# Kernel optimization log

Measured on AMD Instinct MI355X. Metric: run time of the kernel, lower is better.

The kernel has to match this reference:

```python
import jax, jax.numpy as jnp
import numpy as np

NUM_CLASSES = 4
SIGMA_S = 1.0
SIGMA_Z = 1.0


def _rbf_gram(x, sigma):
    # x: [N, d] -> [N, N] Gaussian kernel exp(-||xi-xj||^2 / (2 sigma^2))
    sq = jnp.sum(x * x, axis=-1)
    d2 = sq[:, None] + sq[None, :] - 2.0 * (x @ x.T)
    d2 = jnp.maximum(d2, 0.0)
    return jnp.exp(-d2 / (2.0 * sigma * sigma))


def _double_center(K):
    # Faithful to: K = mean_center(K, dim=0); K_m = mean_center(K.t(), dim=0)
    K = K - jnp.mean(K, axis=0, keepdims=True)
    K = K.T
    K = K - jnp.mean(K, axis=0, keepdims=True)
    return K


def setup_inputs() -> dict:
    key = jax.random.key(0)
    kz, ks = jax.random.split(key)
    z = jax.random.normal(kz, (8192, 128), dtype=jnp.float32)
    s = jax.random.randint(ks, (8192,), 0, NUM_CLASSES, dtype=jnp.int64)
    norm = jnp.float32(1.0)
    return {"z": z, "s": s, "norm": norm}


def reference(z, s, norm):
    n = z.shape[0]
    s_onehot = jax.nn.one_hot(s, NUM_CLASSES, dtype=z.dtype)  # format_onehot
    K_sm = _double_center(_rbf_gram(s_onehot, SIGMA_S))
    K_zm = _double_center(_rbf_gram(z, SIGMA_Z))
    # trace(K_zm.T @ K_sm) == sum(K_zm * K_sm): O(N^2) instead of O(N^3)
    dep = jnp.sum(K_zm * K_sm)
    dep = dep / (norm * (n * n))
    return dep
```

## Files before the change

kernel.cpp:

```cpp
#include <hip/hip_runtime.h>
#include <hip/hip_bf16.h>

typedef short bf16x8 __attribute__((ext_vector_type(8)));
typedef float f32x4  __attribute__((ext_vector_type(4)));

#define ZD      128
#define BT      128
#define D2_CUT  60.0f
#define D2_TRIG 62.0f

__device__ __forceinline__ unsigned short f2bf(float x) {
    unsigned u = __float_as_uint(x);
    u = (u + 0x7FFFu + ((u >> 16) & 1u)) >> 16;
    return (unsigned short)u;
}

__global__ __launch_bounds__(256) void dep_prep(
    const float* __restrict__ z, const int* __restrict__ s,
    float* __restrict__ sq, float* __restrict__ sqmin,
    unsigned short* __restrict__ zb, int* __restrict__ counts)
{
    __shared__ float part[64][33];
    const int tid  = threadIdx.x;
    const int wave = tid >> 6, lane = tid & 63;
    const int half = lane >> 5, c = lane & 31;
    const int r0   = blockIdx.x * 64;

    if (wave == 0) {
        int sv = s[r0 + lane];
        #pragma unroll
        for (int cl = 0; cl < 4; ++cl) {
            unsigned long long m = __ballot(sv == cl);
            if (lane == 0) atomicAdd(&counts[cl], __popcll(m));
        }
    }

    #pragma unroll
    for (int i = 0; i < 8; ++i) {
        const int rloc = wave * 16 + i * 2 + half;
        const int r    = r0 + rloc;
        float4 v = ((const float4*)z)[r * 32 + c];
        ushort4 u;
        u.x = f2bf(v.x); u.y = f2bf(v.y); u.z = f2bf(v.z); u.w = f2bf(v.w);
        ((ushort4*)zb)[r * 32 + c] = u;
        part[rloc][c] = v.x*v.x + v.y*v.y + v.z*v.z + v.w*v.w;
    }
    __syncthreads();

    if (wave == 0) {
        float sum = 0.f;
        #pragma unroll
        for (int k = 0; k < 32; ++k) sum += part[lane][k];
        sq[r0 + lane] = sum;
        float mn = sum;
        #pragma unroll
        for (int off = 1; off < 64; off <<= 1)
            mn = fminf(mn, __shfl_xor(mn, off, 64));
        if (lane == 0) sqmin[blockIdx.x] = mn;
    }
}

__global__ __launch_bounds__(256, 2) void dep_pair(
    const unsigned short* __restrict__ zb, const float* __restrict__ sq,
    const float* __restrict__ sqmin, const int* __restrict__ s,
    const int* __restrict__ counts, float* __restrict__ acc_out,
    int T, float invN)
{
    __shared__ unsigned short Apan[BT * ZD];
    __shared__ unsigned short Bpan[BT * ZD];

    const int tid = threadIdx.x;

    const int t = blockIdx.x;
    #define TRI_BASE(x) ((x) * T - ((x) * ((x) - 1)) / 2)
    double disc = (2.0 * T + 1.0) * (2.0 * T + 1.0) - 8.0 * (double)t;
    int ti = (int)((2.0 * T + 1.0 - sqrt(disc)) * 0.5);
    if (ti < 0) ti = 0;
    if (ti > T - 1) ti = T - 1;
    while (ti + 1 < T && TRI_BASE(ti + 1) <= t) ++ti;
    while (ti > 0 && TRI_BASE(ti) > t) --ti;
    const int tj = ti + (t - TRI_BASE(ti));
    #undef TRI_BASE

    const int i0 = ti * BT, j0 = tj * BT;

    #pragma unroll
    for (int i = 0; i < 8; ++i) {
        const int L   = i * 256 + tid;
        const int row = L >> 4, ch = L & 15;
        const int dst = row * ZD + (((ch ^ (row & 15)) << 3));
        uint4 a = ((const uint4*)(zb + (size_t)i0 * ZD))[L];
        uint4 b = ((const uint4*)(zb + (size_t)j0 * ZD))[L];
        *(uint4*)(Apan + dst) = a;
        *(uint4*)(Bpan + dst) = b;
    }
    __syncthreads();

    const int wave = tid >> 6, lane = tid & 63;
    const int wi = wave >> 1, wj = wave & 1;
    const int l15 = lane & 15, quad = lane >> 4;

    f32x4 accv[4][4];
    #pragma unroll
    for (int a = 0; a < 4; ++a)
        #pragma unroll
        for (int b = 0; b < 4; ++b)
            accv[a][b] = (f32x4){0.f, 0.f, 0.f, 0.f};

    #pragma unroll
    for (int kc = 0; kc < 4; ++kc) {
        bf16x8 af[4], bfr[4];
        #pragma unroll
        for (int it = 0; it < 4; ++it) {
            const int row = wi * 64 + it * 16 + l15;
            const int ch  = (quad + 4 * kc) ^ l15;
            af[it] = *(const bf16x8*)(Apan + row * ZD + (ch << 3));
        }
        #pragma unroll
        for (int jt = 0; jt < 4; ++jt) {
            const int row = wj * 64 + jt * 16 + l15;
            const int ch  = (quad + 4 * kc) ^ l15;
            bfr[jt] = *(const bf16x8*)(Bpan + row * ZD + (ch << 3));
        }
        #pragma unroll
        for (int it = 0; it < 4; ++it)
            #pragma unroll
            for (int jt = 0; jt < 4; ++jt)
                accv[it][jt] = __builtin_amdgcn_mfma_f32_16x16x32_bf16(
                    af[it], bfr[jt], accv[it][jt], 0, 0, 0);
    }

    float m = -1e30f;
    #pragma unroll
    for (int it = 0; it < 4; ++it)
        #pragma unroll
        for (int jt = 0; jt < 4; ++jt) {
            const f32x4 v = accv[it][jt];
            m = fmaxf(m, fmaxf(fmaxf(v[0], v[1]), fmaxf(v[2], v[3])));
        }
    #pragma unroll
    for (int off = 1; off < 64; off <<= 1)
        m = fmaxf(m, __shfl_xor(m, off, 64));

    const int gA = ti * 2 + wi, gB = tj * 2 + wj;
    const float bound = sqmin[gA] + sqmin[gB] - 2.0f * m;

    if (bound < D2_TRIG) {
        float p[4];
        #pragma unroll
        for (int cl = 0; cl < 4; ++cl) p[cl] = (float)counts[cl] * invN;
        const float sump2 = p[0]*p[0] + p[1]*p[1] + p[2]*p[2] + p[3]*p[3];

        const int ibase = i0 + wi * 64, jbase = j0 + wj * 64;
        float sqj[4];
        #pragma unroll
        for (int jt = 0; jt < 4; ++jt) sqj[jt] = sq[jbase + jt * 16 + l15];

        float local = 0.f;
        #pragma unroll
        for (int it = 0; it < 4; ++it) {
            #pragma unroll
            for (int r = 0; r < 4; ++r) {
                const int i = ibase + it * 16 + quad * 4 + r;
                const float sqi = sq[i];
                #pragma unroll
                for (int jt = 0; jt < 4; ++jt) {
                    const int j = jbase + jt * 16 + l15;
                    float d2 = sqi + sqj[jt] - 2.0f * accv[it][jt][r];
                    d2 = fmaxf(d2, 0.0f);
                    if (d2 < D2_CUT && i != j) {
                        const int si = s[i], sj = s[j];
                        const float w = (si == sj ? 1.0f : 0.0f)
                                      - p[si] - p[sj] + sump2;
                        local += w * __expf(-0.5f * d2);
                    }
                }
            }
        }
        if (ti < tj) local *= 2.0f;

        #pragma unroll
        for (int off = 32; off > 0; off >>= 1)
            local += __shfl_down(local, off, 64);
        if (lane == 0 && local != 0.0f)
            atomicAdd(acc_out, local);
    }
}

__global__ __launch_bounds__(64) void dep_finalize(
    const float* __restrict__ acc, const int* __restrict__ counts,
    const float* __restrict__ norm, float* __restrict__ out, int N)
{
    if (threadIdx.x == 0) {
        double n  = (double)N;
        double c2 = 0.0;
        for (int cl = 0; cl < 4; ++cl)
            c2 += (double)counts[cl] * (double)counts[cl];
        double diag  = n - c2 / n;
        double total = ((double)acc[0] + diag) * (1.0 - exp(-1.0));
        out[0] = (float)(total / ((double)norm[0] * n * n));
    }
}

extern "C" void kernel_launch(void* const* d_in, const int* in_sizes, int n_in,
                              void* d_out, int out_size, void* d_ws, size_t ws_size,
                              hipStream_t stream)
{
    const float* z    = (const float*)d_in[0];
    const int*   s    = (const int*)d_in[1];
    const float* norm = (const float*)d_in[2];
    float* out = (float*)d_out;

    const int N = in_sizes[1];
    const int T = N / BT;

    char* ws = (char*)d_ws;
    float* acc    = (float*)ws;
    int*   counts = (int*)(ws + 16);
    float* sq     = (float*)(ws + 64);
    float* sqmin  = (float*)(ws + 64 + (size_t)N * 4);
    unsigned short* zb =
        (unsigned short*)(ws + 64 + (size_t)N * 4 + (size_t)(N / 64) * 4 + 48);

    hipMemsetAsync(d_ws, 0, 64, stream);
    dep_prep<<<N / 64, 256, 0, stream>>>(z, s, sq, sqmin, zb, counts);

    const int nblocks = T * (T + 1) / 2;
    dep_pair<<<nblocks, 256, 0, stream>>>(zb, sq, sqmin, s, counts, acc,
                                          T, 1.0f / (float)N);
    dep_finalize<<<1, 64, 0, stream>>>(acc, counts, norm, out, N);
}
```

Before: 87.11 us.

## Drop A-panel LDS, fuse finalize via last-block counter, remove memset

The pair kernel no longer stages the A tile in shared memory. Each wave loads its A fragments straight from global memory, double-buffered across k-chunks, which halves LDS use and lets launch bounds rise to three blocks per SM. The memset and the finalize kernel are removed: the prep kernel zeroes the accumulator and writes per-block class counts instead of using atomics, and the last pair block, found through an atomic done counter, computes the final value. This saves two launches and LDS pressure, at the cost of uncoalesced global A loads, extra register pressure, and a loop over all per-block counts in every active block.

```diff
diff --git a/kernel.cpp b/kernel.cpp
--- a/kernel.cpp
+++ b/kernel.cpp
@@ -18,7 +18,8 @@
 __global__ __launch_bounds__(256) void dep_prep(
     const float* __restrict__ z, const int* __restrict__ s,
     float* __restrict__ sq, float* __restrict__ sqmin,
-    unsigned short* __restrict__ zb, int* __restrict__ counts)
+    unsigned short* __restrict__ zb, int* __restrict__ counts4,
+    float* __restrict__ acc, unsigned int* __restrict__ done)
 {
     __shared__ float part[64][33];
     const int tid  = threadIdx.x;
@@ -26,12 +27,14 @@
     const int half = lane >> 5, c = lane & 31;
     const int r0   = blockIdx.x * 64;
 
+    if (blockIdx.x == 0 && tid == 192) { *acc = 0.0f; *done = 0u; }
+
     if (wave == 0) {
         int sv = s[r0 + lane];
         #pragma unroll
         for (int cl = 0; cl < 4; ++cl) {
             unsigned long long m = __ballot(sv == cl);
-            if (lane == 0) atomicAdd(&counts[cl], __popcll(m));
+            if (lane == 0) counts4[blockIdx.x * 4 + cl] = __popcll(m);
         }
     }
 
@@ -60,13 +63,14 @@
     }
 }
 
-__global__ __launch_bounds__(256, 2) void dep_pair(
+__global__ __launch_bounds__(256, 3) void dep_pair(
     const unsigned short* __restrict__ zb, const float* __restrict__ sq,
     const float* __restrict__ sqmin, const int* __restrict__ s,
-    const int* __restrict__ counts, float* __restrict__ acc_out,
-    int T, float invN)
+    const int* __restrict__ counts4, int nPrep,
+    float* __restrict__ acc, unsigned int* __restrict__ done,
+    const float* __restrict__ norm, float* __restrict__ out,
+    int T, int N, float invN)
 {
-    __shared__ unsigned short Apan[BT * ZD];
     __shared__ unsigned short Bpan[BT * ZD];
 
     const int tid = threadIdx.x;
@@ -83,22 +87,29 @@
     #undef TRI_BASE
 
     const int i0 = ti * BT, j0 = tj * BT;
+    const int wave = tid >> 6, lane = tid & 63;
+    const int wi = wave >> 1, wj = wave & 1;
+    const int l15 = lane & 15, quad = lane >> 4;
 
     #pragma unroll
     for (int i = 0; i < 8; ++i) {
         const int L   = i * 256 + tid;
         const int row = L >> 4, ch = L & 15;
         const int dst = row * ZD + (((ch ^ (row & 15)) << 3));
-        uint4 a = ((const uint4*)(zb + (size_t)i0 * ZD))[L];
-        uint4 b = ((const uint4*)(zb + (size_t)j0 * ZD))[L];
-        *(uint4*)(Apan + dst) = a;
-        *(uint4*)(Bpan + dst) = b;
-    }
+        *(uint4*)(Bpan + dst) = ((const uint4*)(zb + (size_t)j0 * ZD))[L];
+    }
+
+    const unsigned short* abase[4];
+    #pragma unroll
+    for (int it = 0; it < 4; ++it)
+        abase[it] = zb + (size_t)(i0 + wi * 64 + it * 16 + l15) * ZD + quad * 8;
+
+    bf16x8 af[2][4];
+    #pragma unroll
+    for (int it = 0; it < 4; ++it)
+        af[0][it] = *(const bf16x8*)(abase[it]);
+
     __syncthreads();
-
-    const int wave = tid >> 6, lane = tid & 63;
-    const int wi = wave >> 1, wj = wave & 1;
-    const int l15 = lane & 15, quad = lane >> 4;
 
     f32x4 accv[4][4];
     #pragma unroll
@@ -109,13 +120,13 @@
 
     #pragma unroll
     for (int kc = 0; kc < 4; ++kc) {
-        bf16x8 af[4], bfr[4];
-        #pragma unroll
-        for (int it = 0; it < 4; ++it) {
-            const int row = wi * 64 + it * 16 + l15;
-            const int ch  = (quad + 4 * kc) ^ l15;
-            af[it] = *(const bf16x8*)(Apan + row * ZD + (ch << 3));
-        }
+        if (kc < 3) {
+            #pragma unroll
+            for (int it = 0; it < 4; ++it)
+                af[(kc + 1) & 1][it] =
+                    *(const bf16x8*)(abase[it] + (kc + 1) * 32);
+        }
+        bf16x8 bfr[4];
         #pragma unroll
         for (int jt = 0; jt < 4; ++jt) {
             const int row = wj * 64 + jt * 16 + l15;
@@ -127,7 +138,7 @@
             #pragma unroll
             for (int jt = 0; jt < 4; ++jt)
                 accv[it][jt] = __builtin_amdgcn_mfma_f32_16x16x32_bf16(
-                    af[it], bfr[jt], accv[it][jt], 0, 0, 0);
+                    af[kc & 1][it], bfr[jt], accv[it][jt], 0, 0, 0);
     }
 
     float m = -1e30f;
@@ -146,9 +157,16 @@
     const float bound = sqmin[gA] + sqmin[gB] - 2.0f * m;
 
     if (bound < D2_TRIG) {
+        int cnt[4] = {0, 0, 0, 0};
+        for (int b = 0; b < nPrep; ++b) {
+            cnt[0] += counts4[b * 4 + 0];
+            cnt[1] += counts4[b * 4 + 1];
+            cnt[2] += counts4[b * 4 + 2];
+            cnt[3] += counts4[b * 4 + 3];
+        }
         float p[4];
         #pragma unroll
-        for (int cl = 0; cl < 4; ++cl) p[cl] = (float)counts[cl] * invN;
+        for (int cl = 0; cl < 4; ++cl) p[cl] = (float)cnt[cl] * invN;
         const float sump2 = p[0]*p[0] + p[1]*p[1] + p[2]*p[2] + p[3]*p[3];
 
         const int ibase = i0 + wi * 64, jbase = j0 + wj * 64;
@@ -183,22 +201,25 @@
         for (int off = 32; off > 0; off >>= 1)
             local += __shfl_down(local, off, 64);
         if (lane == 0 && local != 0.0f)
-            atomicAdd(acc_out, local);
-    }
-}
-
-__global__ __launch_bounds__(64) void dep_finalize(
-    const float* __restrict__ acc, const int* __restrict__ counts,
-    const float* __restrict__ norm, float* __restrict__ out, int N)
-{
-    if (threadIdx.x == 0) {
-        double n  = (double)N;
-        double c2 = 0.0;
-        for (int cl = 0; cl < 4; ++cl)
-            c2 += (double)counts[cl] * (double)counts[cl];
-        double diag  = n - c2 / n;
-        double total = ((double)acc[0] + diag) * (1.0 - exp(-1.0));
-        out[0] = (float)(total / ((double)norm[0] * n * n));
+            atomicAdd(acc, local);
+    }
+
+    __syncthreads();
+    if (tid == 0) {
+        __threadfence();
+        if (atomicAdd(done, 1u) == (unsigned)gridDim.x - 1u) {
+            float a = atomicAdd(acc, 0.0f);
+            double c2 = 0.0;
+            for (int cl = 0; cl < 4; ++cl) {
+                long long cc = 0;
+                for (int b = 0; b < nPrep; ++b) cc += counts4[b * 4 + cl];
+                c2 += (double)cc * (double)cc;
+            }
+            double n     = (double)N;
+            double diag  = n - c2 / n;
+            double total = ((double)a + diag) * (1.0 - exp(-1.0));
+            out[0] = (float)(total / ((double)norm[0] * n * n));
+        }
     }
 }
 
@@ -213,20 +234,21 @@
 
     const int N = in_sizes[1];
     const int T = N / BT;
+    const int nPrep = N / 64;
 
     char* ws = (char*)d_ws;
-    float* acc    = (float*)ws;
-    int*   counts = (int*)(ws + 16);
-    float* sq     = (float*)(ws + 64);
-    float* sqmin  = (float*)(ws + 64 + (size_t)N * 4);
-    unsigned short* zb =
-        (unsigned short*)(ws + 64 + (size_t)N * 4 + (size_t)(N / 64) * 4 + 48);
-
-    hipMemsetAsync(d_ws, 0, 64, stream);
-    dep_prep<<<N / 64, 256, 0, stream>>>(z, s, sq, sqmin, zb, counts);
+    float*        acc     = (float*)ws;
+    unsigned int* done    = (unsigned int*)(ws + 8);
+    int*          counts4 = (int*)(ws + 64);
+    float*        sq      = (float*)(ws + 64 + 2048);
+    float*        sqmin   = (float*)(ws + 64 + 2048 + (size_t)N * 4);
+    unsigned short* zb    = (unsigned short*)(ws + 64 + 2048 + (size_t)N * 4
+                                              + (size_t)nPrep * 4);
+
+    dep_prep<<<nPrep, 256, 0, stream>>>(z, s, sq, sqmin, zb, counts4, acc, done);
 
     const int nblocks = T * (T + 1) / 2;
-    dep_pair<<<nblocks, 256, 0, stream>>>(zb, sq, sqmin, s, counts, acc,
-                                          T, 1.0f / (float)N);
-    dep_finalize<<<1, 64, 0, stream>>>(acc, counts, norm, out, N);
-}
+    dep_pair<<<nblocks, 256, 0, stream>>>(zb, sq, sqmin, s, counts4, nPrep,
+                                          acc, done, norm, out,
+                                          T, N, 1.0f / (float)N);
+}
```

After: 142.0 us. 63.1% more time.

## Make pair kernel persistent with register-prefetched tiles and drop memset

Applied to the files above, without the earlier changes.

The pair kernel becomes persistent: 512 blocks loop over the 2080 triangular tiles, and each block prefetches the next tile's panels into registers while it computes the current one. Per-block class counts are written to a small array instead of global atomics, and the accumulator is zeroed inside the prep kernel, so the memset launch is gone. This targets the launch overhead of many short blocks and overlaps global loads with MFMA work, at the cost of more register pressure. It also adds a per-wave reduction of the count array whenever a tile passes the bound test.

```diff
diff --git a/kernel.cpp b/kernel.cpp
--- a/kernel.cpp
+++ b/kernel.cpp
@@ -15,10 +15,41 @@
     return (unsigned short)u;
 }
 
+__device__ __forceinline__ void trimap(int t, int T, int& ti, int& tj) {
+    #define TRI_BASE(x) ((x) * T - ((x) * ((x) - 1)) / 2)
+    double disc = (2.0 * T + 1.0) * (2.0 * T + 1.0) - 8.0 * (double)t;
+    int x = (int)((2.0 * T + 1.0 - sqrt(disc)) * 0.5);
+    if (x < 0) x = 0;
+    if (x > T - 1) x = T - 1;
+    while (x + 1 < T && TRI_BASE(x + 1) <= t) ++x;
+    while (x > 0 && TRI_BASE(x) > t) --x;
+    ti = x;
+    tj = x + (t - TRI_BASE(x));
+    #undef TRI_BASE
+}
+
+__device__ __forceinline__ void sum_counts(const int* counts4, int nPrep,
+                                           int lane, int cnt[4]) {
+    int c0 = 0, c1 = 0, c2 = 0, c3 = 0;
+    for (int b = lane; b < nPrep; b += 64) {
+        const int* p = counts4 + b * 4;
+        c0 += p[0]; c1 += p[1]; c2 += p[2]; c3 += p[3];
+    }
+    #pragma unroll
+    for (int off = 1; off < 64; off <<= 1) {
+        c0 += __shfl_xor(c0, off, 64);
+        c1 += __shfl_xor(c1, off, 64);
+        c2 += __shfl_xor(c2, off, 64);
+        c3 += __shfl_xor(c3, off, 64);
+    }
+    cnt[0] = c0; cnt[1] = c1; cnt[2] = c2; cnt[3] = c3;
+}
+
 __global__ __launch_bounds__(256) void dep_prep(
     const float* __restrict__ z, const int* __restrict__ s,
     float* __restrict__ sq, float* __restrict__ sqmin,
-    unsigned short* __restrict__ zb, int* __restrict__ counts)
+    unsigned short* __restrict__ zb, int* __restrict__ counts4,
+    float* __restrict__ acc)
 {
     __shared__ float part[64][33];
     const int tid  = threadIdx.x;
@@ -26,12 +57,14 @@
     const int half = lane >> 5, c = lane & 31;
     const int r0   = blockIdx.x * 64;
 
+    if (blockIdx.x == 0 && tid == 192) *acc = 0.0f;
+
     if (wave == 0) {
         int sv = s[r0 + lane];
         #pragma unroll
         for (int cl = 0; cl < 4; ++cl) {
             unsigned long long m = __ballot(sv == cl);
-            if (lane == 0) atomicAdd(&counts[cl], __popcll(m));
+            if (lane == 0) counts4[blockIdx.x * 4 + cl] = __popcll(m);
         }
     }
 
@@ -63,139 +96,164 @@
 __global__ __launch_bounds__(256, 2) void dep_pair(
     const unsigned short* __restrict__ zb, const float* __restrict__ sq,
     const float* __restrict__ sqmin, const int* __restrict__ s,
-    const int* __restrict__ counts, float* __restrict__ acc_out,
-    int T, float invN)
+    const int* __restrict__ counts4, int nPrep,
+    float* __restrict__ acc, int T, float invN)
 {
     __shared__ unsigned short Apan[BT * ZD];
     __shared__ unsigned short Bpan[BT * ZD];
 
-    const int tid = threadIdx.x;
-
-    const int t = blockIdx.x;
-    #define TRI_BASE(x) ((x) * T - ((x) * ((x) - 1)) / 2)
-    double disc = (2.0 * T + 1.0) * (2.0 * T + 1.0) - 8.0 * (double)t;
-    int ti = (int)((2.0 * T + 1.0 - sqrt(disc)) * 0.5);
-    if (ti < 0) ti = 0;
-    if (ti > T - 1) ti = T - 1;
-    while (ti + 1 < T && TRI_BASE(ti + 1) <= t) ++ti;
-    while (ti > 0 && TRI_BASE(ti) > t) --ti;
-    const int tj = ti + (t - TRI_BASE(ti));
-    #undef TRI_BASE
-
-    const int i0 = ti * BT, j0 = tj * BT;
-
-    #pragma unroll
-    for (int i = 0; i < 8; ++i) {
-        const int L   = i * 256 + tid;
-        const int row = L >> 4, ch = L & 15;
-        const int dst = row * ZD + (((ch ^ (row & 15)) << 3));
-        uint4 a = ((const uint4*)(zb + (size_t)i0 * ZD))[L];
-        uint4 b = ((const uint4*)(zb + (size_t)j0 * ZD))[L];
-        *(uint4*)(Apan + dst) = a;
-        *(uint4*)(Bpan + dst) = b;
-    }
-    __syncthreads();
-
+    const int tid  = threadIdx.x;
     const int wave = tid >> 6, lane = tid & 63;
     const int wi = wave >> 1, wj = wave & 1;
     const int l15 = lane & 15, quad = lane >> 4;
-
-    f32x4 accv[4][4];
-    #pragma unroll
-    for (int a = 0; a < 4; ++a)
-        #pragma unroll
-        for (int b = 0; b < 4; ++b)
-            accv[a][b] = (f32x4){0.f, 0.f, 0.f, 0.f};
-
-    #pragma unroll
-    for (int kc = 0; kc < 4; ++kc) {
-        bf16x8 af[4], bfr[4];
-        #pragma unroll
-        for (int it = 0; it < 4; ++it) {
-            const int row = wi * 64 + it * 16 + l15;
-            const int ch  = (quad + 4 * kc) ^ l15;
-            af[it] = *(const bf16x8*)(Apan + row * ZD + (ch << 3));
-        }
-        #pragma unroll
-        for (int jt = 0; jt < 4; ++jt) {
-            const int row = wj * 64 + jt * 16 + l15;
-            const int ch  = (quad + 4 * kc) ^ l15;
-            bfr[jt] = *(const bf16x8*)(Bpan + row * ZD + (ch << 3));
-        }
+    const int NT = T * (T + 1) / 2;
+
+    int t = blockIdx.x;
+    if (t >= NT) return;
+
+    int ti, tj;
+    trimap(t, T, ti, tj);
+
+    uint4 ra[8], rb[8];
+    {
+        const uint4* pa = (const uint4*)(zb + (size_t)ti * BT * ZD);
+        const uint4* pb = (const uint4*)(zb + (size_t)tj * BT * ZD);
+        #pragma unroll
+        for (int i = 0; i < 8; ++i) {
+            ra[i] = pa[i * 256 + tid];
+            rb[i] = pb[i * 256 + tid];
+        }
+    }
+
+    while (t < NT) {
+        const int cti = ti, ctj = tj;
+        const int i0 = cti * BT, j0 = ctj * BT;
+
+        #pragma unroll
+        for (int i = 0; i < 8; ++i) {
+            const int L   = i * 256 + tid;
+            const int row = L >> 4, ch = L & 15;
+            const int dst = row * ZD + (((ch ^ (row & 15))) << 3);
+            *(uint4*)(Apan + dst) = ra[i];
+            *(uint4*)(Bpan + dst) = rb[i];
+        }
+        __syncthreads();
+
+        const int tn = t + gridDim.x;
+        if (tn < NT) {
+            trimap(tn, T, ti, tj);
+            const uint4* pa = (const uint4*)(zb + (size_t)ti * BT * ZD);
+            const uint4* pb = (const uint4*)(zb + (size_t)tj * BT * ZD);
+            #pragma unroll
+            for (int i = 0; i < 8; ++i) {
+                ra[i] = pa[i * 256 + tid];
+                rb[i] = pb[i * 256 + tid];
+            }
+        }
+
+        f32x4 accv[4][4];
+        #pragma unroll
+        for (int a = 0; a < 4; ++a)
+            #pragma unroll
+            for (int b = 0; b < 4; ++b)
+                accv[a][b] = (f32x4){0.f, 0.f, 0.f, 0.f};
+
+        #pragma unroll
+        for (int kc = 0; kc < 4; ++kc) {
+            bf16x8 af[4], bfr[4];
+            const int ch = (quad + 4 * kc) ^ l15;
+            #pragma unroll
+            for (int it = 0; it < 4; ++it) {
+                const int row = wi * 64 + it * 16 + l15;
+                af[it] = *(const bf16x8*)(Apan + row * ZD + (ch << 3));
+            }
+            #pragma unroll
+            for (int jt = 0; jt < 4; ++jt) {
+                const int row = wj * 64 + jt * 16 + l15;
+                bfr[jt] = *(const bf16x8*)(Bpan + row * ZD + (ch << 3));
+            }
+            #pragma unroll
+            for (int it = 0; it < 4; ++it)
+                #pragma unroll
+                for (int jt = 0; jt < 4; ++jt)
+                    accv[it][jt] = __builtin_amdgcn_mfma_f32_16x16x32_bf16(
+                        af[it], bfr[jt], accv[it][jt], 0, 0, 0);
+        }
+
+        float m = -1e30f;
         #pragma unroll
         for (int it = 0; it < 4; ++it)
             #pragma unroll
-            for (int jt = 0; jt < 4; ++jt)
-                accv[it][jt] = __builtin_amdgcn_mfma_f32_16x16x32_bf16(
-                    af[it], bfr[jt], accv[it][jt], 0, 0, 0);
-    }
-
-    float m = -1e30f;
-    #pragma unroll
-    for (int it = 0; it < 4; ++it)
-        #pragma unroll
-        for (int jt = 0; jt < 4; ++jt) {
-            const f32x4 v = accv[it][jt];
-            m = fmaxf(m, fmaxf(fmaxf(v[0], v[1]), fmaxf(v[2], v[3])));
-        }
-    #pragma unroll
-    for (int off = 1; off < 64; off <<= 1)
-        m = fmaxf(m, __shfl_xor(m, off, 64));
-
-    const int gA = ti * 2 + wi, gB = tj * 2 + wj;
-    const float bound = sqmin[gA] + sqmin[gB] - 2.0f * m;
-
-    if (bound < D2_TRIG) {
-        float p[4];
-        #pragma unroll
-        for (int cl = 0; cl < 4; ++cl) p[cl] = (float)counts[cl] * invN;
-        const float sump2 = p[0]*p[0] + p[1]*p[1] + p[2]*p[2] + p[3]*p[3];
-
-        const int ibase = i0 + wi * 64, jbase = j0 + wj * 64;
-        float sqj[4];
-        #pragma unroll
-        for (int jt = 0; jt < 4; ++jt) sqj[jt] = sq[jbase + jt * 16 + l15];
-
-        float local = 0.f;
-        #pragma unroll
-        for (int it = 0; it < 4; ++it) {
-            #pragma unroll
-            for (int r = 0; r < 4; ++r) {
-                const int i = ibase + it * 16 + quad * 4 + r;
-                const float sqi = sq[i];
+            for (int jt = 0; jt < 4; ++jt) {
+                const f32x4 v = accv[it][jt];
+                m = fmaxf(m, fmaxf(fmaxf(v[0], v[1]), fmaxf(v[2], v[3])));
+            }
+        #pragma unroll
+        for (int off = 1; off < 64; off <<= 1)
+            m = fmaxf(m, __shfl_xor(m, off, 64));
+
+        const float bound = sqmin[cti * 2 + wi] + sqmin[ctj * 2 + wj] - 2.0f * m;
+
+        if (bound < D2_TRIG) {
+            int cnt[4];
+            sum_counts(counts4, nPrep, lane, cnt);
+            float p[4];
+            #pragma unroll
+            for (int cl = 0; cl < 4; ++cl) p[cl] = (float)cnt[cl] * invN;
+            const float sump2 = p[0]*p[0] + p[1]*p[1] + p[2]*p[2] + p[3]*p[3];
+
+            const int ibase = i0 + wi * 64, jbase = j0 + wj * 64;
+            float sqj[4];
+            #pragma unroll
+            for (int jt = 0; jt < 4; ++jt) sqj[jt] = sq[jbase + jt * 16 + l15];
+
+            float local = 0.f;
+            #pragma unroll
+            for (int it = 0; it < 4; ++it) {
                 #pragma unroll
-                for (int jt = 0; jt < 4; ++jt) {
-                    const int j = jbase + jt * 16 + l15;
-                    float d2 = sqi + sqj[jt] - 2.0f * accv[it][jt][r];
-                    d2 = fmaxf(d2, 0.0f);
-                    if (d2 < D2_CUT && i != j) {
-                        const int si = s[i], sj = s[j];
-                        const float w = (si == sj ? 1.0f : 0.0f)
-                                      - p[si] - p[sj] + sump2;
-                        local += w * __expf(-0.5f * d2);
+                for (int r = 0; r < 4; ++r) {
+                    const int i = ibase + it * 16 + quad * 4 + r;
+                    const float sqi = sq[i];
+                    #pragma unroll
+                    for (int jt = 0; jt < 4; ++jt) {
+                        const int j = jbase + jt * 16 + l15;
+                        float d2 = sqi + sqj[jt] - 2.0f * accv[it][jt][r];
+                        d2 = fmaxf(d2, 0.0f);
+                        if (d2 < D2_CUT && i != j) {
+                            const int si = s[i], sj = s[j];
+                            const float w = (si == sj ? 1.0f : 0.0f)
+                                          - p[si] - p[sj] + sump2;
+                            local += w * __expf(-0.5f * d2);
+                        }
                     }
                 }
             }
-        }
-        if (ti < tj) local *= 2.0f;
-
-        #pragma unroll
-        for (int off = 32; off > 0; off >>= 1)
-            local += __shfl_down(local, off, 64);
-        if (lane == 0 && local != 0.0f)
-            atomicAdd(acc_out, local);
+            if (cti < ctj) local *= 2.0f;
+
+            #pragma unroll
+            for (int off = 32; off > 0; off >>= 1)
+                local += __shfl_down(local, off, 64);
+            if (lane == 0 && local != 0.0f)
+                atomicAdd(acc, local);
+        }
+
+        __syncthreads();
+        t = tn;
     }
 }
 
 __global__ __launch_bounds__(64) void dep_finalize(
-    const float* __restrict__ acc, const int* __restrict__ counts,
+    const float* __restrict__ acc, const int* __restrict__ counts4, int nPrep,
     const float* __restrict__ norm, float* __restrict__ out, int N)
 {
-    if (threadIdx.x == 0) {
+    const int lane = threadIdx.x & 63;
+    int cnt[4];
+    sum_counts(counts4, nPrep, lane, cnt);
+    if (lane == 0) {
         double n  = (double)N;
         double c2 = 0.0;
         for (int cl = 0; cl < 4; ++cl)
-            c2 += (double)counts[cl] * (double)counts[cl];
+            c2 += (double)cnt[cl] * (double)cnt[cl];
         double diag  = n - c2 / n;
         double total = ((double)acc[0] + diag) * (1.0 - exp(-1.0));
         out[0] = (float)(total / ((double)norm[0] * n * n));
@@ -213,20 +271,18 @@
 
     const int N = in_sizes[1];
     const int T = N / BT;
+    const int nPrep = N / 64;
 
     char* ws = (char*)d_ws;
-    float* acc    = (float*)ws;
-    int*   counts = (int*)(ws + 16);
-    float* sq     = (float*)(ws + 64);
-    float* sqmin  = (float*)(ws + 64 + (size_t)N * 4);
-    unsigned short* zb =
-        (unsigned short*)(ws + 64 + (size_t)N * 4 + (size_t)(N / 64) * 4 + 48);
-
-    hipMemsetAsync(d_ws, 0, 64, stream);
-    dep_prep<<<N / 64, 256, 0, stream>>>(z, s, sq, sqmin, zb, counts);
-
-    const int nblocks = T * (T + 1) / 2;
-    dep_pair<<<nblocks, 256, 0, stream>>>(zb, sq, sqmin, s, counts, acc,
-                                          T, 1.0f / (float)N);
-    dep_finalize<<<1, 64, 0, stream>>>(acc, counts, norm, out, N);
-}
+    float*        acc     = (float*)ws;
+    int*          counts4 = (int*)(ws + 64);
+    float*        sq      = (float*)(ws + 64 + 2048);
+    float*        sqmin   = (float*)(ws + 64 + 2048 + (size_t)N * 4);
+    unsigned short* zb    = (unsigned short*)(ws + 64 + 2048 + (size_t)N * 4
+                                              + (size_t)nPrep * 4);
+
+    dep_prep<<<nPrep, 256, 0, stream>>>(z, s, sq, sqmin, zb, counts4, acc);
+    dep_pair<<<512, 256, 0, stream>>>(zb, sq, sqmin, s, counts4, nPrep,
+                                      acc, T, 1.0f / (float)N);
+    dep_finalize<<<1, 64, 0, stream>>>(acc, counts4, nPrep, norm, out, N);
+}
```

Measured after the change: 113.6 us. +30.5%, slower.
